# Performance work log

Measured on AMD Instinct MI355X. Metric: run time of the kernel, lower is better.

## Reference

```python
import jax, jax.numpy as jnp
import numpy as np

N_NODES = 50000
N_EDGES = 1600000
F_IN, F_HID, F_MID = 264, 48, 64


def setup_inputs() -> dict:
    key = jax.random.key(0)
    ks = jax.random.split(key, 12)
    def lin(kw, fan_in, fan_out):
        s = 1.0 / np.sqrt(fan_in)
        return jax.random.uniform(kw, (fan_in, fan_out), jnp.float32, -s, s)
    return {
        "x": jax.random.normal(ks[0], (N_NODES, F_IN), jnp.float32),
        "edge_index": jax.random.randint(ks[1], (2, N_EDGES), 0, N_NODES, jnp.int64),
        "edge_weight": jax.random.uniform(ks[2], (N_EDGES,), jnp.float32, 0.01, 1.0),
        "WM": lin(ks[3], F_IN, F_HID), "bM": jnp.zeros((F_HID,), jnp.float32),
        "WA": lin(ks[4], F_IN, F_HID), "bA": jnp.zeros((F_HID,), jnp.float32),
        "WS": lin(ks[5], F_IN, F_HID), "bS": jnp.zeros((F_HID,), jnp.float32),
        "W1": lin(ks[6], 3 * F_HID, F_MID), "b1": jnp.zeros((F_MID,), jnp.float32),
        "W2": lin(ks[7], F_MID, 1), "b2": jnp.zeros((1,), jnp.float32),
    }


def _gcn_norm(edge_index, edge_weight, n):
    # add self-loops with weight 1 (PyG gcn_norm default)
    loop = jnp.arange(n, dtype=edge_index.dtype)
    row = jnp.concatenate([edge_index[0], loop])
    col = jnp.concatenate([edge_index[1], loop])
    w = jnp.concatenate([edge_weight, jnp.ones((n,), edge_weight.dtype)])
    deg = jax.ops.segment_sum(w, col, num_segments=n)
    dis = jnp.where(deg > 0, jax.lax.rsqrt(jnp.where(deg > 0, deg, 1.0)), 0.0)
    norm = dis[row] * w * dis[col]
    return row, col, norm


def reference(x, edge_index, edge_weight, WM, bM, WA, bA, WS, bS, W1, b1, W2, b2):
    n = x.shape[0]
    row, col, norm = _gcn_norm(edge_index, edge_weight, n)

    # GCNConv aggr='max': linear (no bias) -> gather -> weighted scatter-max -> +bias
    hM = x @ WM                              # [N, 48]
    msgM = norm[:, None] * hM[row]           # [E+N, 48]
    outM = jax.ops.segment_max(msgM, col, num_segments=n) + bM
    xConvM = jax.nn.relu(outM)

    # GCNConv aggr='add'
    hA = x @ WA
    msgA = norm[:, None] * hA[row]
    outA = jax.ops.segment_sum(msgA, col, num_segments=n) + bA
    xConvA = jax.nn.relu(outA)

    # plain linear branch
    xLin = jax.nn.relu(x @ WS + bS)

    h = jnp.concatenate([xConvM, xConvA, xLin], axis=1)  # [N, 144]
    h = jax.nn.relu(h @ W1 + b1)
    out = h @ W2 + b2                         # [N, 1]
    return out.squeeze(-1)
```

## Files before the change

### kernel.cpp

```cpp
#include <hip/hip_runtime.h>
#include <stdint.h>

#define N_NODES 50000
#define N_EDGES 1600000
#define F_IN    264
#define F_HID   48
#define F_CAT   144
#define F_MID   64
#define K_PAD   288
#define K_MLP   160

#define BSH     6
#define NB      782
#define NBP     1024
#define CHUNK   2048
#define NCHUNK  ((N_EDGES + CHUNK - 1) / CHUNK)
#define SCAN_BLOCKS ((NB * 64 + 255) / 256)

typedef unsigned short u16;
typedef unsigned int   u32;

using short8  = __attribute__((ext_vector_type(8))) short;
using floatx4 = __attribute__((ext_vector_type(4))) float;
using floatx2 = __attribute__((ext_vector_type(2))) float;
using uintx4  = __attribute__((ext_vector_type(4))) u32;

__device__ __forceinline__ float bf2f(u16 u) {
    return __uint_as_float(((u32)u) << 16);
}
__device__ __forceinline__ u16 f2bf(float f) {
    u32 u = __float_as_uint(f);
    u32 r = (u + 0x7fffu + ((u >> 16) & 1u)) >> 16;
    return (u16)r;
}
__device__ __forceinline__ float ldf(const void* p, size_t i, int isbf) {
    return isbf ? bf2f(((const u16*)p)[i]) : ((const float*)p)[i];
}
__device__ __forceinline__ uintx4 s8_to_u4(short8 v) {
    union { short8 s; uintx4 u; } c; c.s = v; return c.u;
}

__device__ __forceinline__ int ld_row(const int* ei, int e, int is64) {
    return is64 ? ei[2 * (size_t)e] : ei[e];
}
__device__ __forceinline__ int ld_col(const int* ei, int e, int is64) {
    return is64 ? ei[2 * ((size_t)N_EDGES + e)] : ei[(size_t)N_EDGES + e];
}

__global__ __launch_bounds__(256)
void k_prep(const void* __restrict__ WM, const void* __restrict__ WA,
            const void* __restrict__ WS, const void* __restrict__ W1,
            const void* __restrict__ bM, const void* __restrict__ bA,
            const void* __restrict__ b1, const void* __restrict__ W2,
            const void* __restrict__ b2,
            u16* __restrict__ Wt, u16* __restrict__ W1bt,
            float* __restrict__ bMf, float* __restrict__ bAf,
            float* __restrict__ b1f, float* __restrict__ W2f,
            float* __restrict__ b2f,
            const u16* __restrict__ xu, const int* __restrict__ ei,
            int* __restrict__ flags, u32* __restrict__ cnt) {
    __shared__ int sfl[2];
    const int tid = threadIdx.x;
    if (tid < 64) {
        u16 h = xu[2 * tid];
        u32 E = (h >> 7) & 0xFF;
        int sane = (h == 0) || (E >= 90 && E <= 140);
        unsigned long long m = __ballot(sane);
        int z = (tid < 16) ? ei[2 * tid + 1] : 0;
        unsigned long long nz = __ballot(z != 0);
        if (tid == 0) {
            sfl[0] = (__popcll(m) >= 48) ? 1 : 0;
            sfl[1] = (nz == 0ull) ? 1 : 0;
        }
    }
    __syncthreads();
    const int isbf = sfl[0];
    if (blockIdx.x == 0 && tid == 0) {
        flags[0] = sfl[0]; flags[1] = sfl[1]; cnt[0] = 0u;
    }
    int t = blockIdx.x * 256 + tid;
    if (t < F_CAT * K_PAD) {
        int n = t / K_PAD, k = t - n * K_PAD;
        u16 v = 0;
        if (k < F_IN) {
            const void* W = (n < 48) ? WM : (n < 96) ? WA : WS;
            int nn = (n < 48) ? n : (n < 96) ? n - 48 : n - 96;
            if (isbf) v = ((const u16*)W)[(size_t)k * 48 + nn];
            else      v = f2bf(((const float*)W)[(size_t)k * 48 + nn]);
        }
        Wt[(size_t)n * K_PAD + k] = v;
        return;
    }
    t -= F_CAT * K_PAD;
    if (t < F_MID * K_MLP) {
        int j = t / K_MLP, k = t - j * K_MLP;
        u16 v = 0;
        if (k < F_CAT) {
            if (isbf) v = ((const u16*)W1)[(size_t)k * F_MID + j];
            else      v = f2bf(((const float*)W1)[(size_t)k * F_MID + j]);
        }
        W1bt[t] = v;
        return;
    }
    t -= F_MID * K_MLP;
    if (t < 48)            { bMf[t] = ldf(bM, t, isbf); return; }
    t -= 48;
    if (t < 48)            { bAf[t] = ldf(bA, t, isbf); return; }
    t -= 48;
    if (t < 64)            { b1f[t] = ldf(b1, t, isbf); return; }
    t -= 64;
    if (t < 64)            { W2f[t] = ldf(W2, t, isbf); return; }
    t -= 64;
    if (t < 1)             { b2f[0] = ldf(b2, 0, isbf); return; }
}

__global__ __launch_bounds__(256)
void k_bhist(const int* __restrict__ ei, u32* __restrict__ bhist,
             const int* __restrict__ flags) {
    const int is64 = flags[1];
    __shared__ u32 hist[NB];
    for (int j = threadIdx.x; j < NB; j += 256) hist[j] = 0;
    __syncthreads();
    int e0 = blockIdx.x * CHUNK;
    for (int i = 0; i < CHUNK / 256; ++i) {
        int e = e0 + i * 256 + threadIdx.x;
        if (e < N_EDGES) {
            int c = ld_col(ei, e, is64);
            atomicAdd(&hist[(u32)c >> BSH], 1u);
        }
    }
    __syncthreads();
    for (int j = threadIdx.x; j < NB; j += 256)
        bhist[(size_t)j * NCHUNK + blockIdx.x] = hist[j];
}

__global__ __launch_bounds__(256)
void k_bscan(u32* __restrict__ bhist, u32* __restrict__ bsum,
             u32* __restrict__ boff, u32* __restrict__ cnt) {
    const int tid  = threadIdx.x;
    const int wid  = (blockIdx.x * 256 + tid) >> 6;
    const int lane = tid & 63;
    __shared__ int lastFlag;
    __shared__ u32 wsum2[4];
    if (wid < NB) {
        u32* row = bhist + (size_t)wid * NCHUNK;
        u32 run = 0;
        for (int i0 = 0; i0 < NCHUNK; i0 += 64) {
            int i = i0 + lane;
            u32 v = (i < NCHUNK) ? row[i] : 0u;
            u32 sc = v;
#pragma unroll
            for (int off = 1; off < 64; off <<= 1) {
                u32 t2 = (u32)__shfl_up((int)sc, off, 64);
                if (lane >= off) sc += t2;
            }
            if (i < NCHUNK) row[i] = run + sc - v;
            run += (u32)__shfl((int)sc, 63, 64);
        }
        if (lane == 0)
            __hip_atomic_store(&bsum[wid], run, __ATOMIC_RELAXED,
                               __HIP_MEMORY_SCOPE_AGENT);
    }
    __syncthreads();
    if (tid == 0) {
        __threadfence();
        u32 old = __hip_atomic_fetch_add(cnt, 1u, __ATOMIC_ACQ_REL,
                                         __HIP_MEMORY_SCOPE_AGENT);
        lastFlag = (old == (u32)(SCAN_BLOCKS - 1));
    }
    __syncthreads();
    if (!lastFlag) return;
    u32 a[4];
#pragma unroll
    for (int u = 0; u < 4; ++u) {
        int i = 4 * tid + u;
        a[u] = (i < NB) ? __hip_atomic_load(&bsum[i], __ATOMIC_RELAXED,
                                            __HIP_MEMORY_SCOPE_AGENT) : 0u;
    }
    u32 s = a[0] + a[1] + a[2] + a[3];
    u32 sc = s;
#pragma unroll
    for (int off = 1; off < 64; off <<= 1) {
        u32 t2 = (u32)__shfl_up((int)sc, off, 64);
        if ((tid & 63) >= off) sc += t2;
    }
    if ((tid & 63) == 63) wsum2[tid >> 6] = sc;
    __syncthreads();
    u32 wbase = 0;
    for (int wv = 0; wv < (tid >> 6); ++wv) wbase += wsum2[wv];
    u32 excl = wbase + sc - s;
    int i0 = 4 * tid;
    u32 b0 = excl, b1 = excl + a[0], b2 = excl + a[0] + a[1],
        b3 = excl + a[0] + a[1] + a[2];
    if (i0     <= NB) boff[i0]     = b0;
    if (i0 + 1 <= NB) boff[i0 + 1] = b1;
    if (i0 + 2 <= NB) boff[i0 + 2] = b2;
    if (i0 + 3 <= NB) boff[i0 + 3] = b3;
}

__global__ __launch_bounds__(256)
void k_bplace(const int* __restrict__ ei, const void* __restrict__ ew,
              const u32* __restrict__ bhist, const u32* __restrict__ boff,
              int2* __restrict__ bpair, const int* __restrict__ flags) {
    const int isbf = flags[0], is64 = flags[1];
    const int blk = blockIdx.x;
    const int tid = threadIdx.x;
    __shared__ int2 stage[CHUNK];
    __shared__ u32 lcur[NBP];
    __shared__ u32 lbase[NBP];
    __shared__ u32 wsum[4];
    for (int j = tid; j < NBP; j += 256) lcur[j] = 0;
    __syncthreads();
    const int e0 = blk * CHUNK;
    u32 cv[CHUNK / 256];
#pragma unroll
    for (int i = 0; i < CHUNK / 256; ++i) {
        int e = e0 + i * 256 + tid;
        u32 c = 0xFFFFFFFFu;
        if (e < N_EDGES) {
            c = (u32)ld_col(ei, e, is64);
            atomicAdd(&lcur[c >> BSH], 1u);
        }
        cv[i] = c;
    }
    __syncthreads();
    {
        u32 a0 = lcur[4 * tid], a1 = lcur[4 * tid + 1];
        u32 a2 = lcur[4 * tid + 2], a3 = lcur[4 * tid + 3];
        u32 s = a0 + a1 + a2 + a3;
        u32 sc = s;
        int lane = tid & 63;
#pragma unroll
        for (int off = 1; off < 64; off <<= 1) {
            u32 t = (u32)__shfl_up((int)sc, off, 64);
            if (lane >= off) sc += t;
        }
        if (lane == 63) wsum[tid >> 6] = sc;
        __syncthreads();
        u32 wbase = 0;
        for (int wv = 0; wv < (tid >> 6); ++wv) wbase += wsum[wv];
        u32 excl = wbase + sc - s;
        lbase[4 * tid]     = excl;
        lbase[4 * tid + 1] = excl + a0;
        lbase[4 * tid + 2] = excl + a0 + a1;
        lbase[4 * tid + 3] = excl + a0 + a1 + a2;
        __syncthreads();
        lcur[4 * tid]     = excl;
        lcur[4 * tid + 1] = excl + a0;
        lcur[4 * tid + 2] = excl + a0 + a1;
        lcur[4 * tid + 3] = excl + a0 + a1 + a2;
    }
    __syncthreads();
#pragma unroll
    for (int i = 0; i < CHUNK / 256; ++i) {
        if (cv[i] != 0xFFFFFFFFu) {
            int e = e0 + i * 256 + tid;
            u32 c = cv[i];
            u32 j = c >> BSH;
            int r = ld_row(ei, e, is64);
            float w = ldf(ew, e, isbf);
            u32 slot = atomicAdd(&lcur[j], 1u);
            stage[slot] = make_int2(r | (int)((c & 63u) << 16) | (int)(j << 22),
                                    __float_as_int(w));
        }
    }
    __syncthreads();
    int tot = N_EDGES - e0; if (tot > CHUNK) tot = CHUNK;
    for (int i = tid; i < tot; i += 256) {
        int2 e2 = stage[i];
        u32 j = (u32)e2.x >> 22;
        u32 tgt = boff[j] + bhist[(size_t)j * NCHUNK + blk] + ((u32)i - lbase[j]);
        bpair[tgt] = e2;
    }
}

__global__ __launch_bounds__(256)
void k_bcsr(const int2* __restrict__ bpair, const u32* __restrict__ boff,
            int* __restrict__ rowptr, int2* __restrict__ csr_pair,
            float* __restrict__ dis) {
    const int b   = blockIdx.x;
    const int tid = threadIdx.x;
    const u32 base = boff[b];
    const u32 n    = boff[b + 1] - base;
    const int c0   = b << BSH;
    __shared__ u32 chist[64], pcur[64], pbeg[64];
    if (tid < 64) chist[tid] = 0;
    __syncthreads();
    for (u32 i = tid; i < n; i += 256)
        atomicAdd(&chist[((u32)bpair[base + i].x >> 16) & 63u], 1u);
    __syncthreads();
    if (tid < 64) {
        u32 v = chist[tid];
        u32 sc = v;
        for (int off = 1; off < 64; off <<= 1) {
            u32 t = (u32)__shfl_up((int)sc, off, 64);
            if (tid >= off) sc += t;
        }
        u32 excl = sc - v;
        pcur[tid] = excl;
        pbeg[tid] = excl;
        int c = c0 + tid;
        if (c <= N_NODES) rowptr[c] = (int)(base + excl);
    }
    __syncthreads();
    for (u32 i = tid; i < n; i += 256) {
        int2 e2 = bpair[base + i];
        u32 lc = ((u32)e2.x >> 16) & 63u;
        u32 lr = atomicAdd(&pcur[lc], 1u);
        csr_pair[base + lr] = make_int2(e2.x & 0xFFFF, e2.y);
    }
    __syncthreads();
    int j = tid >> 2, sub = tid & 3;
    int c = c0 + j;
    if (c < N_NODES) {
        u32 s0 = base + pbeg[j], s1 = base + pcur[j];
        float s = 0.f;
        for (u32 i = s0 + sub; i < s1; i += 4)
            s += __int_as_float(csr_pair[i].y);
        s += __shfl_down(s, 2, 4);
        s += __shfl_down(s, 1, 4);
        if (sub == 0) dis[c] = rsqrtf(1.0f + s);
    }
}

__global__ __launch_bounds__(256)
void k_gemm(const void* __restrict__ x, const u16* __restrict__ Wt,
            u16* __restrict__ hMB, u16* __restrict__ hFull,
            const void* __restrict__ bS, const int* __restrict__ flags) {
    const int isbf = flags[0];
    const int lane = threadIdx.x & 63;
    const int wave = threadIdx.x >> 6;
    const int mrow = lane & 15;
    const int q    = lane >> 4;
    const int m_base = blockIdx.x * 128 + wave * 32;

    floatx4 acc[2][9];
#pragma unroll
    for (int tt = 0; tt < 2; ++tt)
#pragma unroll
        for (int t = 0; t < 9; ++t) {
            acc[tt][t][0]=0.f; acc[tt][t][1]=0.f; acc[tt][t][2]=0.f; acc[tt][t][3]=0.f;
        }

    for (int k0 = 0; k0 < K_PAD; k0 += 32) {
        int k = k0 + q * 8;
        short8 a[2];
#pragma unroll
        for (int tt = 0; tt < 2; ++tt) {
            int node = m_base + tt * 16 + mrow;
            short8 av = {0,0,0,0,0,0,0,0};
            if (node < N_NODES && k < F_IN) {
                if (isbf) {
                    av = *(const short8*)((const u16*)x + (size_t)node * F_IN + k);
                } else {
                    const float* xf = (const float*)x + (size_t)node * F_IN + k;
                    floatx4 v0 = *(const floatx4*)xf;
                    floatx4 v1 = *(const floatx4*)(xf + 4);
                    av[0]=(short)f2bf(v0[0]); av[1]=(short)f2bf(v0[1]);
                    av[2]=(short)f2bf(v0[2]); av[3]=(short)f2bf(v0[3]);
                    av[4]=(short)f2bf(v1[0]); av[5]=(short)f2bf(v1[1]);
                    av[6]=(short)f2bf(v1[2]); av[7]=(short)f2bf(v1[3]);
                }
            }
            a[tt] = av;
        }
#pragma unroll
        for (int t = 0; t < 9; ++t) {
            short8 b = *(const short8*)(Wt + (size_t)(t * 16 + mrow) * K_PAD + k);
            acc[0][t] = __builtin_amdgcn_mfma_f32_16x16x32_bf16(a[0], b, acc[0][t], 0, 0, 0);
            acc[1][t] = __builtin_amdgcn_mfma_f32_16x16x32_bf16(a[1], b, acc[1][t], 0, 0, 0);
        }
    }
#pragma unroll
    for (int tt = 0; tt < 2; ++tt)
#pragma unroll
    for (int t = 0; t < 9; ++t) {
        int n = t * 16 + mrow;
#pragma unroll
        for (int r = 0; r < 4; ++r) {
            int row = m_base + tt * 16 + q * 4 + r;
            if (row < N_NODES) {
                float v = acc[tt][t][r];
                if (n < 96) hMB[(size_t)row * 96 + n] = f2bf(v);
                else        hFull[(size_t)row * F_CAT + n] =
                                f2bf(fmaxf(v + ldf(bS, n - 96, isbf), 0.f));
            }
        }
    }
}

__global__ __launch_bounds__(256)
void k_agg(const u16* __restrict__ hMB, u16* __restrict__ hFull,
           const int* __restrict__ rowptr, const int2* __restrict__ csr_pair,
           const float* __restrict__ dis,
           const float* __restrict__ bMf, const float* __restrict__ bAf) {
    const int lane = threadIdx.x & 63;
    const int wave = threadIdx.x >> 6;
    const int node = blockIdx.x * 4 + wave;

    const int g = lane / 12;
    const int s = lane - g * 12;
    const bool active = lane < 60;
    const bool isMax = s < 6;

    const int start = rowptr[node];
    const int end   = rowptr[node + 1];
    const float dn  = dis[node];
    const float dn2 = dn * dn;
    const float padnm = isMax ? dn2 : 0.f;

    const u32 s16     = 16u * (u32)s;
    const u32 selfOff = __umul24((u32)node, 192u) + s16;

    floatx2 acc2[4];
    {
        short8 rv0 = *(const short8*)((const char*)hMB + selfOff);
        uintx4 w4 = s8_to_u4(rv0);
        float seed = (isMax || g == 0) ? dn2 : 0.f;
#pragma unroll
        for (int p = 0; p < 4; ++p) {
            acc2[p][0] = seed * __uint_as_float(w4[p] << 16);
            acc2[p][1] = seed * __uint_as_float(w4[p] & 0xffff0000u);
        }
    }

    for (int c0 = start; c0 < end; c0 += 64) {
        int cl = end - c0; if (cl > 64) cl = 64;
        int li = lane < cl ? lane : cl - 1;
        int2 mp = csr_pair[c0 + li];
        float disr = dis[mp.x];
        float mynm = __int_as_float(mp.y) * disr * dn;
        u32 myoff  = __umul24((u32)mp.x, 192u);

        for (int j = 0; j < cl; j += 20) {
            u32 offv[4]; float nmv[4];
#pragma unroll
            for (int u = 0; u < 4; ++u) {
                int el = j + 5 * u + g;
                bool valid = active && (el < cl);
                int elc = (el < cl) ? el : 0;
                u32 off  = (u32)__shfl((int)myoff, elc, 64) + s16;
                float nm = __shfl(mynm, elc, 64);
                offv[u] = valid ? off : selfOff;
                nmv[u]  = valid ? nm  : padnm;
            }
            short8 rv[4];
#pragma unroll
            for (int u = 0; u < 4; ++u)
                rv[u] = *(const short8*)((const char*)hMB + offv[u]);
#pragma unroll
            for (int u = 0; u < 4; ++u) {
                uintx4 w4 = s8_to_u4(rv[u]);
                floatx2 nm2; nm2[0] = nmv[u]; nm2[1] = nmv[u];
#pragma unroll
                for (int p = 0; p < 4; ++p) {
                    floatx2 f;
                    f[0] = __uint_as_float(w4[p] << 16);
                    f[1] = __uint_as_float(w4[p] & 0xffff0000u);
                    if (isMax) {
                        floatx2 m = nm2 * f;
                        acc2[p][0] = fmaxf(acc2[p][0], m[0]);
                        acc2[p][1] = fmaxf(acc2[p][1], m[1]);
                    } else {
                        acc2[p] += nm2 * f;
                    }
                }
            }
        }
    }

#pragma unroll
    for (int gg = 1; gg < 5; ++gg) {
        int src = lane + 12 * gg;
        floatx2 t[4];
#pragma unroll
        for (int p = 0; p < 4; ++p) {
            t[p][0] = __shfl(acc2[p][0], src, 64);
            t[p][1] = __shfl(acc2[p][1], src, 64);
        }
        if (lane < 12) {
            if (isMax) {
#pragma unroll
                for (int p = 0; p < 4; ++p) {
                    acc2[p][0] = fmaxf(acc2[p][0], t[p][0]);
                    acc2[p][1] = fmaxf(acc2[p][1], t[p][1]);
                }
            } else {
#pragma unroll
                for (int p = 0; p < 4; ++p) acc2[p] += t[p];
            }
        }
    }

    if (lane < 12) {
        const float* bp = isMax ? (bMf + 8 * lane) : (bAf + 8 * lane - 48);
        short8 hv;
#pragma unroll
        for (int p = 0; p < 4; ++p) {
            hv[2 * p]     = (short)f2bf(fmaxf(acc2[p][0] + bp[2 * p],     0.f));
            hv[2 * p + 1] = (short)f2bf(fmaxf(acc2[p][1] + bp[2 * p + 1], 0.f));
        }
        *(short8*)(hFull + (size_t)node * F_CAT + 8 * lane) = hv;
    }
}

__global__ __launch_bounds__(256)
void k_mlp(const u16* __restrict__ hFull, const u16* __restrict__ W1bt,
           const float* __restrict__ b1f, const float* __restrict__ W2f,
           const float* __restrict__ b2f, void* __restrict__ out,
           const int* __restrict__ flags) {
    const int isbf = flags[0];
    const int lane = threadIdx.x & 63;
    const int wave = threadIdx.x >> 6;
    const int mrow = lane & 15;
    const int q    = lane >> 4;
    const int m_base = blockIdx.x * 64 + wave * 16;
    const int node = m_base + mrow;

    floatx4 acc[4];
#pragma unroll
    for (int t = 0; t < 4; ++t) { acc[t][0]=0.f; acc[t][1]=0.f; acc[t][2]=0.f; acc[t][3]=0.f; }

    for (int k0 = 0; k0 < K_MLP; k0 += 32) {
        int k = k0 + q * 8;
        short8 a = {0,0,0,0,0,0,0,0};
        if (node < N_NODES && k < F_CAT)
            a = *(const short8*)(hFull + (size_t)node * F_CAT + k);
#pragma unroll
        for (int t = 0; t < 4; ++t) {
            short8 b = *(const short8*)(W1bt + (size_t)(t * 16 + mrow) * K_MLP + k);
            acc[t] = __builtin_amdgcn_mfma_f32_16x16x32_bf16(a, b, acc[t], 0, 0, 0);
        }
    }

    float pr[4] = {0.f, 0.f, 0.f, 0.f};
#pragma unroll
    for (int t = 0; t < 4; ++t) {
        int n = t * 16 + mrow;
        float b1v = b1f[n], w2v = W2f[n];
#pragma unroll
        for (int r = 0; r < 4; ++r)
            pr[r] += fmaxf(acc[t][r] + b1v, 0.f) * w2v;
    }
#pragma unroll
    for (int mask = 1; mask < 16; mask <<= 1)
#pragma unroll
        for (int r = 0; r < 4; ++r) pr[r] += __shfl_xor(pr[r], mask, 64);
    if (mrow == 0) {
#pragma unroll
        for (int r = 0; r < 4; ++r) {
            int nd = m_base + q * 4 + r;
            if (nd < N_NODES) {
                float res = pr[r] + b2f[0];
                if (isbf) ((u16*)out)[nd] = f2bf(res);
                else      ((float*)out)[nd] = res;
            }
        }
    }
}

extern "C" void kernel_launch(void* const* d_in, const int* in_sizes, int n_in,
                              void* d_out, int out_size, void* d_ws, size_t ws_size,
                              hipStream_t stream) {
    const void* x  = d_in[0];
    const int*  ei = (const int*)d_in[1];
    const void* ew = d_in[2];
    const void* WM = d_in[3];
    const void* bM = d_in[4];
    const void* WA = d_in[5];
    const void* bA = d_in[6];
    const void* WS = d_in[7];
    const void* bS = d_in[8];
    const void* W1 = d_in[9];
    const void* b1 = d_in[10];
    const void* W2 = d_in[11];
    const void* b2 = d_in[12];

    char* p = (char*)d_ws;
    auto alloc = [&](size_t bytes) -> char* {
        char* r = p; p += (bytes + 255) & ~(size_t)255; return r;
    };
    int*   flags    = (int*)  alloc(16);
    u32*   cnt      = (u32*)  alloc(16);
    float* dis      = (float*)alloc((size_t)N_NODES * 4);
    int*   rowptr   = (int*)  alloc((size_t)(N_NODES + 1) * 4);
    int2*  csr_pair = (int2*) alloc((size_t)N_EDGES * 8);
    u16*   hMB      = (u16*)  alloc((size_t)N_NODES * 96 * 2);
    u16*   hFull    = (u16*)  alloc((size_t)N_NODES * F_CAT * 2);
    u16*   Wt       = (u16*)  alloc((size_t)F_CAT * K_PAD * 2);
    u16*   W1bt    = (u16*)  alloc((size_t)F_MID * K_MLP * 2);
    u32*   bhist    = (u32*)  alloc((size_t)NB * NCHUNK * 4);
    u32*   bsum     = (u32*)  alloc((size_t)NB * 4);
    u32*   boff     = (u32*)  alloc((size_t)(NB + 1) * 4);
    float* bMf      = (float*)alloc(48 * 4);
    float* bAf      = (float*)alloc(48 * 4);
    float* b1f      = (float*)alloc(64 * 4);
    float* W2f      = (float*)alloc(64 * 4);
    float* b2f      = (float*)alloc(4);
    int2*  bpair    = (int2*)hMB;

    k_prep  <<<(F_CAT * K_PAD + F_MID * K_MLP + 225 + 255) / 256, 256, 0, stream>>>(
                 WM, WA, WS, W1, bM, bA, b1, W2, b2,
                 Wt, W1bt, bMf, bAf, b1f, W2f, b2f,
                 (const u16*)x, ei, flags, cnt);
    k_bhist <<<NCHUNK, 256, 0, stream>>>(ei, bhist, flags);
    k_bscan <<<SCAN_BLOCKS, 256, 0, stream>>>(bhist, bsum, boff, cnt);
    k_bplace<<<NCHUNK, 256, 0, stream>>>(ei, ew, bhist, boff, bpair, flags);
    k_bcsr  <<<NB, 256, 0, stream>>>(bpair, boff, rowptr, csr_pair, dis);
    k_gemm  <<<(N_NODES + 127) / 128, 256, 0, stream>>>(x, Wt, hMB, hFull, bS, flags);
    k_agg   <<<N_NODES / 4, 256, 0, stream>>>(hMB, hFull, rowptr, csr_pair, dis, bMf, bAf);
    k_mlp   <<<(N_NODES + 63) / 64, 256, 0, stream>>>(hFull, W1bt, b1f, W2f, b2f, d_out, flags);
    (void)in_sizes; (void)n_in; (void)out_size; (void)ws_size;
}
```

Measured before the change: 265.3 us.

## Shrink GEMM wave tile, accumulate degree via LDS atomics, double bucketing chunk

The GEMM kernel now gives each wave a single 16-row tile instead of two, halving the accumulator registers and doubling the grid, to raise occupancy. The CSR build kernel sums edge weights per column with shared-memory float atomics during placement, which removes a second pass that re-read csr_pair. The bucketing chunk size goes from 2048 to 4096, halving the number of histogram blocks and the size of the scan. The costs are that each weight fragment is reused across fewer rows, there is LDS atomic contention on dsum, and float summation order becomes nondeterministic.

```diff
diff --git a/kernel.cpp b/kernel.cpp
--- a/kernel.cpp
+++ b/kernel.cpp
@@ -13,7 +13,7 @@
 #define BSH     6
 #define NB      782
 #define NBP     1024
-#define CHUNK   2048
+#define CHUNK   4096
 #define NCHUNK  ((N_EDGES + CHUNK - 1) / CHUNK)
 #define SCAN_BLOCKS ((NB * 64 + 255) / 256)
 
@@ -283,8 +283,9 @@
     const u32 base = boff[b];
     const u32 n    = boff[b + 1] - base;
     const int c0   = b << BSH;
-    __shared__ u32 chist[64], pcur[64], pbeg[64];
-    if (tid < 64) chist[tid] = 0;
+    __shared__ u32 chist[64], pcur[64];
+    __shared__ float dsum[64];
+    if (tid < 64) { chist[tid] = 0u; dsum[tid] = 0.f; }
     __syncthreads();
     for (u32 i = tid; i < n; i += 256)
         atomicAdd(&chist[((u32)bpair[base + i].x >> 16) & 63u], 1u);
@@ -298,7 +299,6 @@
         }
         u32 excl = sc - v;
         pcur[tid] = excl;
-        pbeg[tid] = excl;
         int c = c0 + tid;
         if (c <= N_NODES) rowptr[c] = (int)(base + excl);
     }
@@ -308,18 +308,12 @@
         u32 lc = ((u32)e2.x >> 16) & 63u;
         u32 lr = atomicAdd(&pcur[lc], 1u);
         csr_pair[base + lr] = make_int2(e2.x & 0xFFFF, e2.y);
-    }
-    __syncthreads();
-    int j = tid >> 2, sub = tid & 3;
-    int c = c0 + j;
-    if (c < N_NODES) {
-        u32 s0 = base + pbeg[j], s1 = base + pcur[j];
-        float s = 0.f;
-        for (u32 i = s0 + sub; i < s1; i += 4)
-            s += __int_as_float(csr_pair[i].y);
-        s += __shfl_down(s, 2, 4);
-        s += __shfl_down(s, 1, 4);
-        if (sub == 0) dis[c] = rsqrtf(1.0f + s);
+        atomicAdd(&dsum[lc], __int_as_float(e2.y));
+    }
+    __syncthreads();
+    if (tid < 64) {
+        int c = c0 + tid;
+        if (c < N_NODES) dis[c] = rsqrtf(1.0f + dsum[tid]);
     }
 }
 
@@ -332,55 +326,45 @@
     const int wave = threadIdx.x >> 6;
     const int mrow = lane & 15;
     const int q    = lane >> 4;
-    const int m_base = blockIdx.x * 128 + wave * 32;
-
-    floatx4 acc[2][9];
-#pragma unroll
-    for (int tt = 0; tt < 2; ++tt)
-#pragma unroll
-        for (int t = 0; t < 9; ++t) {
-            acc[tt][t][0]=0.f; acc[tt][t][1]=0.f; acc[tt][t][2]=0.f; acc[tt][t][3]=0.f;
-        }
+    const int m_base = blockIdx.x * 64 + wave * 16;
+    const int node = m_base + mrow;
+
+    floatx4 acc[9];
+#pragma unroll
+    for (int t = 0; t < 9; ++t) {
+        acc[t][0]=0.f; acc[t][1]=0.f; acc[t][2]=0.f; acc[t][3]=0.f;
+    }
 
     for (int k0 = 0; k0 < K_PAD; k0 += 32) {
         int k = k0 + q * 8;
-        short8 a[2];
-#pragma unroll
-        for (int tt = 0; tt < 2; ++tt) {
-            int node = m_base + tt * 16 + mrow;
-            short8 av = {0,0,0,0,0,0,0,0};
-            if (node < N_NODES && k < F_IN) {
-                if (isbf) {
-                    av = *(const short8*)((const u16*)x + (size_t)node * F_IN + k);
-                } else {
-                    const float* xf = (const float*)x + (size_t)node * F_IN + k;
-                    floatx4 v0 = *(const floatx4*)xf;
-                    floatx4 v1 = *(const floatx4*)(xf + 4);
-                    av[0]=(short)f2bf(v0[0]); av[1]=(short)f2bf(v0[1]);
-                    av[2]=(short)f2bf(v0[2]); av[3]=(short)f2bf(v0[3]);
-                    av[4]=(short)f2bf(v1[0]); av[5]=(short)f2bf(v1[1]);
-                    av[6]=(short)f2bf(v1[2]); av[7]=(short)f2bf(v1[3]);
-                }
-            }
-            a[tt] = av;
+        short8 a = {0,0,0,0,0,0,0,0};
+        if (node < N_NODES && k < F_IN) {
+            if (isbf) {
+                a = *(const short8*)((const u16*)x + (size_t)node * F_IN + k);
+            } else {
+                const float* xf = (const float*)x + (size_t)node * F_IN + k;
+                floatx4 v0 = *(const floatx4*)xf;
+                floatx4 v1 = *(const floatx4*)(xf + 4);
+                a[0]=(short)f2bf(v0[0]); a[1]=(short)f2bf(v0[1]);
+                a[2]=(short)f2bf(v0[2]); a[3]=(short)f2bf(v0[3]);
+                a[4]=(short)f2bf(v1[0]); a[5]=(short)f2bf(v1[1]);
+                a[6]=(short)f2bf(v1[2]); a[7]=(short)f2bf(v1[3]);
+            }
         }
 #pragma unroll
         for (int t = 0; t < 9; ++t) {
             short8 b = *(const short8*)(Wt + (size_t)(t * 16 + mrow) * K_PAD + k);
-            acc[0][t] = __builtin_amdgcn_mfma_f32_16x16x32_bf16(a[0], b, acc[0][t], 0, 0, 0);
-            acc[1][t] = __builtin_amdgcn_mfma_f32_16x16x32_bf16(a[1], b, acc[1][t], 0, 0, 0);
-        }
-    }
-#pragma unroll
-    for (int tt = 0; tt < 2; ++tt)
+            acc[t] = __builtin_amdgcn_mfma_f32_16x16x32_bf16(a, b, acc[t], 0, 0, 0);
+        }
+    }
 #pragma unroll
     for (int t = 0; t < 9; ++t) {
         int n = t * 16 + mrow;
 #pragma unroll
         for (int r = 0; r < 4; ++r) {
-            int row = m_base + tt * 16 + q * 4 + r;
+            int row = m_base + q * 4 + r;
             if (row < N_NODES) {
-                float v = acc[tt][t][r];
+                float v = acc[t][r];
                 if (n < 96) hMB[(size_t)row * 96 + n] = f2bf(v);
                 else        hFull[(size_t)row * F_CAT + n] =
                                 f2bf(fmaxf(v + ldf(bS, n - 96, isbf), 0.f));
@@ -607,7 +591,7 @@
     k_bscan <<<SCAN_BLOCKS, 256, 0, stream>>>(bhist, bsum, boff, cnt);
     k_bplace<<<NCHUNK, 256, 0, stream>>>(ei, ew, bhist, boff, bpair, flags);
     k_bcsr  <<<NB, 256, 0, stream>>>(bpair, boff, rowptr, csr_pair, dis);
-    k_gemm  <<<(N_NODES + 127) / 128, 256, 0, stream>>>(x, Wt, hMB, hFull, bS, flags);
+    k_gemm  <<<(N_NODES + 63) / 64, 256, 0, stream>>>(x, Wt, hMB, hFull, bS, flags);
     k_agg   <<<N_NODES / 4, 256, 0, stream>>>(hMB, hFull, rowptr, csr_pair, dis, bMf, bAf);
     k_mlp   <<<(N_NODES + 63) / 64, 256, 0, stream>>>(hFull, W1bt, b1f, W2f, b2f, d_out, flags);
     (void)in_sizes; (void)n_in; (void)out_size; (void)ws_size;
```

After: 277.3 us. 1.05x slower.
